# Optimization experiments

Measured on AMD Instinct MI355X. Metric: run time of the kernel, lower is better.

## Reference

```python
import jax, jax.numpy as jnp
import numpy as np
import math

CODE_DIMS = [32, 32]
NUM_CODEBOOK = 16
FEAT_DIM = 1024
EPS = 1e-12


def rms_norm(x, eps=EPS):
    var = jnp.mean(x * x, axis=-1, keepdims=True) + eps
    return x * jax.lax.rsqrt(var)


def outer_product(y, code_dims):
    # y: [..., h, sum(code_dims)] -> [..., h, prod(code_dims)]
    splits = list(np.cumsum(code_dims)[:-1])
    mats = jnp.split(y, splits, axis=-1)
    out = mats[0]
    for m in mats[1:]:
        out = out[..., :, None] * m[..., None, :]
        out = out.reshape(*out.shape[:-2], -1)
    return out


def setup_inputs() -> dict:
    key = jax.random.key(0)
    kx, kw = jax.random.split(key)
    x = jax.random.normal(kx, (4, 2048, FEAT_DIM), dtype=jnp.float32)
    std = math.sqrt(2.0 / (FEAT_DIM + sum(CODE_DIMS)))
    weight = jax.random.normal(kw, (NUM_CODEBOOK, FEAT_DIM, sum(CODE_DIMS)), dtype=jnp.float32) * std
    return {"x": x, "weight": weight}


def reference(x, weight):
    h = weight.shape[0]
    # batched per-codebook linear: [..., d] x [h, d, o] -> [..., h, o]
    y = jnp.einsum('...i,hio->...ho', x, weight)
    # chunked outer product per codebook -> [..., h, prod(code_dims)]
    op = outer_product(y, CODE_DIMS)
    out = jnp.mean(op, axis=-2) * math.sqrt(h)
    return rms_norm(out)
```

## Files before the change

### kernel.cpp

```cpp
#include <hip/hip_runtime.h>
#include <hip/hip_bf16.h>

#define NTOK  8192
#define KDIM  1024
#define NOUT  1024
#define NCB   16

typedef __attribute__((ext_vector_type(8))) short short8;
typedef __attribute__((ext_vector_type(4))) float f32x4;

__device__ static inline unsigned short f2bf(float f) {
    unsigned int u = __float_as_uint(f);
    unsigned int r = (u + 0x7FFFu + ((u >> 16) & 1u)) >> 16;
    return (unsigned short)r;
}

__device__ static inline float bf2f(unsigned int h) {
    return __uint_as_float(h << 16);
}

__device__ static inline void async_copy16(const void* g, void* l) {
    __builtin_amdgcn_global_load_lds(
        (const __attribute__((address_space(1))) void*)g,
        (__attribute__((address_space(3))) void*)l, 16, 0, 0);
}

__global__ __launch_bounds__(256) void conv_x_kernel(const float* __restrict__ x,
                                                     unsigned short* __restrict__ A) {
    int u = blockIdx.x * 256 + threadIdx.x;
    const float* src = x + (size_t)u * 8;
    float4 v0 = *(const float4*)(src);
    float4 v1 = *(const float4*)(src + 4);
    short8 o;
    o[0] = (short)f2bf(v0.x); o[1] = (short)f2bf(v0.y);
    o[2] = (short)f2bf(v0.z); o[3] = (short)f2bf(v0.w);
    o[4] = (short)f2bf(v1.x); o[5] = (short)f2bf(v1.y);
    o[6] = (short)f2bf(v1.z); o[7] = (short)f2bf(v1.w);
    *(short8*)(A + (size_t)u * 8) = o;
}

__global__ __launch_bounds__(256) void conv_w_kernel(const float* __restrict__ W,
                                                     unsigned short* __restrict__ Bt) {
    int u = blockIdx.x * 256 + threadIdx.x;
    int n  = u & (NOUT - 1);
    int k0 = (u >> 10) << 3;
    int h = n >> 6, o = n & 63;
    const float* src = W + (size_t)h * KDIM * 64 + o;
    short8 v;
#pragma unroll
    for (int j = 0; j < 8; ++j)
        v[j] = (short)f2bf(src[(size_t)(k0 + j) * 64]);
    *(short8*)(Bt + (size_t)n * KDIM + k0) = v;
}

__global__ __launch_bounds__(256) void gemm_kernel(const unsigned short* __restrict__ A,
                                                   const unsigned short* __restrict__ Bt,
                                                   unsigned short* __restrict__ Y) {
    __shared__ unsigned short Alds[128 * 32];
    __shared__ unsigned short Blds[128 * 32];

    const int tid = threadIdx.x;
    const int m0 = blockIdx.y * 128;
    const int n0 = blockIdx.x * 128;
    const int lane = tid & 63;
    const int w = tid >> 6;
    const int wr = (w >> 1) * 64;
    const int wc = (w & 1) * 64;
    const int r15 = lane & 15;
    const int kq = (lane >> 4) * 8;

    f32x4 acc[4][4];
#pragma unroll
    for (int m = 0; m < 4; ++m)
#pragma unroll
        for (int n = 0; n < 4; ++n)
            acc[m][n] = (f32x4){0.f, 0.f, 0.f, 0.f};

    const unsigned short* Ag = A + (size_t)m0 * KDIM;
    const unsigned short* Bg = Bt + (size_t)n0 * KDIM;

    for (int kt = 0; kt < KDIM; kt += 32) {
#pragma unroll
        for (int issue = 0; issue < 2; ++issue) {
            int e = (issue * 256 + tid) * 8;
            int row = e >> 5;
            int kk = e & 31;
            async_copy16(Ag + (size_t)row * KDIM + kt + kk, Alds + e);
            async_copy16(Bg + (size_t)row * KDIM + kt + kk, Blds + e);
        }
        __syncthreads();

        short8 af[4], bf[4];
#pragma unroll
        for (int m = 0; m < 4; ++m)
            af[m] = *(const short8*)&Alds[(wr + m * 16 + r15) * 32 + kq];
#pragma unroll
        for (int n = 0; n < 4; ++n)
            bf[n] = *(const short8*)&Blds[(wc + n * 16 + r15) * 32 + kq];

#pragma unroll
        for (int m = 0; m < 4; ++m)
#pragma unroll
            for (int n = 0; n < 4; ++n)
                acc[m][n] = __builtin_amdgcn_mfma_f32_16x16x32_bf16(af[m], bf[n], acc[m][n], 0, 0, 0);
        __syncthreads();
    }

    const int rrow = (lane >> 4) * 4;
#pragma unroll
    for (int m = 0; m < 4; ++m) {
#pragma unroll
        for (int n = 0; n < 4; ++n) {
            int col = n0 + wc + n * 16 + r15;
#pragma unroll
            for (int r = 0; r < 4; ++r) {
                int row = m0 + wr + m * 16 + rrow + r;
                Y[(size_t)row * NOUT + col] = f2bf(acc[m][n][r]);
            }
        }
    }
}

__global__ __launch_bounds__(256) void epilogue_kernel(const unsigned short* __restrict__ Y,
                                                       float* __restrict__ out) {
    __shared__ float ylds[1024];
    __shared__ float red[4];

    const int t = blockIdx.x;
    const int tid = threadIdx.x;
    const unsigned short* yrow = Y + (size_t)t * NOUT;

    {
        uint2 raw = *(const uint2*)(yrow + tid * 4);
        ylds[tid * 4 + 0] = bf2f(raw.x & 0xffffu);
        ylds[tid * 4 + 1] = bf2f(raw.x >> 16);
        ylds[tid * 4 + 2] = bf2f(raw.y & 0xffffu);
        ylds[tid * 4 + 3] = bf2f(raw.y >> 16);
    }
    __syncthreads();

    const int j = tid >> 3;
    const int k0 = (tid & 7) * 4;

    float o0 = 0.f, o1 = 0.f, o2 = 0.f, o3 = 0.f;
#pragma unroll
    for (int h = 0; h < NCB; ++h) {
        float a = ylds[h * 64 + j];
        float4 b = *(const float4*)&ylds[h * 64 + 32 + k0];
        o0 += a * b.x; o1 += a * b.y; o2 += a * b.z; o3 += a * b.w;
    }
    o0 *= 0.25f; o1 *= 0.25f; o2 *= 0.25f; o3 *= 0.25f;

    float ss = o0 * o0 + o1 * o1 + o2 * o2 + o3 * o3;
#pragma unroll
    for (int off = 32; off >= 1; off >>= 1)
        ss += __shfl_xor(ss, off, 64);

    const int lane = tid & 63, w = tid >> 6;
    if (lane == 0) red[w] = ss;
    __syncthreads();
    float tot = red[0] + red[1] + red[2] + red[3];
    float scale = rsqrtf(tot * (1.0f / 1024.0f) + 1e-12f);

    float4 o;
    o.x = o0 * scale; o.y = o1 * scale; o.z = o2 * scale; o.w = o3 * scale;
    *(float4*)(out + (size_t)t * 1024 + tid * 4) = o;
}

extern "C" void kernel_launch(void* const* d_in, const int* in_sizes, int n_in,
                              void* d_out, int out_size, void* d_ws, size_t ws_size,
                              hipStream_t stream) {
    const float* x = (const float*)d_in[0];
    const float* wgt = (const float*)d_in[1];
    float* out = (float*)d_out;

    unsigned short* A  = (unsigned short*)d_ws;
    unsigned short* Bt = (unsigned short*)((char*)d_ws + (16u << 20));
    unsigned short* Y  = (unsigned short*)((char*)d_ws + (18u << 20));

    conv_x_kernel<<<NTOK * KDIM / 8 / 256, 256, 0, stream>>>(x, A);
    conv_w_kernel<<<NOUT * KDIM / 8 / 256, 256, 0, stream>>>(wgt, Bt);
    gemm_kernel<<<dim3(NOUT / 128, NTOK / 128), 256, 0, stream>>>(A, Bt, Y);
    epilogue_kernel<<<NTOK, 256, 0, stream>>>(Y, out);
}
```

Measured before the change: 57.51 us.

## Fuse x conversion, GEMM and outer-product epilogue into one full-width kernel

Replaces the separate x-to-bf16 conversion, tiled GEMM and per-token epilogue with one kernel. Each block computes a 32-token by full-1024-column tile with the B operand double-buffered and XOR-swizzled in LDS, and converts x to bf16 on the fly. The fp32 result stays in LDS for the codebook outer-product mean and RMS norm, which removes the Y round trip through global memory and two launches. In exchange it uses 132KB of LDS per block, giving one block per CU and only 256 blocks, and every block re-streams the whole B matrix from L2.

```diff
diff --git a/kernel.cpp b/kernel.cpp
--- a/kernel.cpp
+++ b/kernel.cpp
@@ -1,42 +1,24 @@
 #include <hip/hip_runtime.h>
 #include <hip/hip_bf16.h>
 
-#define NTOK  8192
 #define KDIM  1024
 #define NOUT  1024
-#define NCB   16
+#define MTILE 32
+#define BK    32
+#define YPAD  1028
 
 typedef __attribute__((ext_vector_type(8))) short short8;
 typedef __attribute__((ext_vector_type(4))) float f32x4;
 
 __device__ static inline unsigned short f2bf(float f) {
     unsigned int u = __float_as_uint(f);
-    unsigned int r = (u + 0x7FFFu + ((u >> 16) & 1u)) >> 16;
-    return (unsigned short)r;
-}
-
-__device__ static inline float bf2f(unsigned int h) {
-    return __uint_as_float(h << 16);
+    return (unsigned short)((u + 0x7FFFu + ((u >> 16) & 1u)) >> 16);
 }
 
 __device__ static inline void async_copy16(const void* g, void* l) {
     __builtin_amdgcn_global_load_lds(
         (const __attribute__((address_space(1))) void*)g,
         (__attribute__((address_space(3))) void*)l, 16, 0, 0);
-}
-
-__global__ __launch_bounds__(256) void conv_x_kernel(const float* __restrict__ x,
-                                                     unsigned short* __restrict__ A) {
-    int u = blockIdx.x * 256 + threadIdx.x;
-    const float* src = x + (size_t)u * 8;
-    float4 v0 = *(const float4*)(src);
-    float4 v1 = *(const float4*)(src + 4);
-    short8 o;
-    o[0] = (short)f2bf(v0.x); o[1] = (short)f2bf(v0.y);
-    o[2] = (short)f2bf(v0.z); o[3] = (short)f2bf(v0.w);
-    o[4] = (short)f2bf(v1.x); o[5] = (short)f2bf(v1.y);
-    o[6] = (short)f2bf(v1.z); o[7] = (short)f2bf(v1.w);
-    *(short8*)(A + (size_t)u * 8) = o;
 }
 
 __global__ __launch_bounds__(256) void conv_w_kernel(const float* __restrict__ W,
@@ -53,133 +35,172 @@
     *(short8*)(Bt + (size_t)n * KDIM + k0) = v;
 }
 
-__global__ __launch_bounds__(256) void gemm_kernel(const unsigned short* __restrict__ A,
-                                                   const unsigned short* __restrict__ Bt,
-                                                   unsigned short* __restrict__ Y) {
-    __shared__ unsigned short Alds[128 * 32];
-    __shared__ unsigned short Blds[128 * 32];
-
-    const int tid = threadIdx.x;
-    const int m0 = blockIdx.y * 128;
-    const int n0 = blockIdx.x * 128;
+__device__ static inline void stage_b(const unsigned short* __restrict__ Bt,
+                                      unsigned short* Bl, int tid, int kt) {
+#pragma unroll
+    for (int i = 0; i < 8; ++i) {
+        int slot  = i * 512 + tid;
+        int row   = slot >> 2;
+        int kksrc = (((slot & 3) ^ ((row >> 1) & 3)) << 3);
+        async_copy16(Bt + (size_t)row * KDIM + kt + kksrc, Bl + (size_t)slot * 8);
+    }
+}
+
+__global__ __launch_bounds__(512) void fused_kernel(const float* __restrict__ x,
+                                                    const unsigned short* __restrict__ Bt,
+                                                    float* __restrict__ out) {
+    extern __shared__ char smem[];
+    unsigned short* Bl = (unsigned short*)smem;
+    unsigned short* Al = (unsigned short*)(smem + 131072);
+    float* ylds = (float*)smem;
+
+    const int tid  = threadIdx.x;
+    const int m0   = blockIdx.x * MTILE;
     const int lane = tid & 63;
-    const int w = tid >> 6;
-    const int wr = (w >> 1) * 64;
-    const int wc = (w & 1) * 64;
-    const int r15 = lane & 15;
-    const int kq = (lane >> 4) * 8;
-
-    f32x4 acc[4][4];
-#pragma unroll
-    for (int m = 0; m < 4; ++m)
-#pragma unroll
-        for (int n = 0; n < 4; ++n)
-            acc[m][n] = (f32x4){0.f, 0.f, 0.f, 0.f};
-
-    const unsigned short* Ag = A + (size_t)m0 * KDIM;
-    const unsigned short* Bg = Bt + (size_t)n0 * KDIM;
-
-    for (int kt = 0; kt < KDIM; kt += 32) {
-#pragma unroll
-        for (int issue = 0; issue < 2; ++issue) {
-            int e = (issue * 256 + tid) * 8;
-            int row = e >> 5;
-            int kk = e & 31;
-            async_copy16(Ag + (size_t)row * KDIM + kt + kk, Alds + e);
-            async_copy16(Bg + (size_t)row * KDIM + kt + kk, Blds + e);
+    const int w    = tid >> 6;
+    const int r15  = lane & 15;
+    const int kq   = (lane >> 4) * 8;
+    const int cl   = kq >> 3;
+
+    f32x4 acc[2][8];
+#pragma unroll
+    for (int mi = 0; mi < 2; ++mi)
+#pragma unroll
+        for (int nf = 0; nf < 8; ++nf)
+            acc[mi][nf] = (f32x4){0.f, 0.f, 0.f, 0.f};
+
+    const bool aload = (tid < 128);
+    const int arow = tid >> 2;
+    const int akk  = (tid & 3) * 8;
+    const float* xsrc = x + (size_t)(m0 + arow) * KDIM + akk;
+
+    stage_b(Bt, Bl, tid, 0);
+    if (aload) {
+        float4 v0 = *(const float4*)xsrc;
+        float4 v1 = *(const float4*)(xsrc + 4);
+        short8 o;
+        o[0]=(short)f2bf(v0.x); o[1]=(short)f2bf(v0.y); o[2]=(short)f2bf(v0.z); o[3]=(short)f2bf(v0.w);
+        o[4]=(short)f2bf(v1.x); o[5]=(short)f2bf(v1.y); o[6]=(short)f2bf(v1.z); o[7]=(short)f2bf(v1.w);
+        *(short8*)(Al + arow * 32 + akk) = o;
+    }
+    __syncthreads();
+
+    for (int t = 0; t < 32; ++t) {
+        const int b = t & 1;
+        float4 v0, v1;
+        if (t < 31) {
+            stage_b(Bt, Bl + (b ^ 1) * 32768, tid, (t + 1) * BK);
+            if (aload) {
+                v0 = *(const float4*)(xsrc + (t + 1) * BK);
+                v1 = *(const float4*)(xsrc + (t + 1) * BK + 4);
+            }
+        }
+        short8 af[2], bfr[8];
+        const unsigned short* Ab = Al + b * 1024;
+        const unsigned short* Bb = Bl + b * 32768;
+#pragma unroll
+        for (int mi = 0; mi < 2; ++mi)
+            af[mi] = *(const short8*)(Ab + (mi * 16 + r15) * 32 + kq);
+#pragma unroll
+        for (int nf = 0; nf < 8; ++nf) {
+            int row  = w * 128 + nf * 16 + r15;
+            int phys = ((cl ^ ((row >> 1) & 3)) << 3);
+            bfr[nf] = *(const short8*)(Bb + row * 32 + phys);
+        }
+#pragma unroll
+        for (int mi = 0; mi < 2; ++mi)
+#pragma unroll
+            for (int nf = 0; nf < 8; ++nf)
+                acc[mi][nf] = __builtin_amdgcn_mfma_f32_16x16x32_bf16(af[mi], bfr[nf], acc[mi][nf], 0, 0, 0);
+        if (t < 31 && aload) {
+            short8 o;
+            o[0]=(short)f2bf(v0.x); o[1]=(short)f2bf(v0.y); o[2]=(short)f2bf(v0.z); o[3]=(short)f2bf(v0.w);
+            o[4]=(short)f2bf(v1.x); o[5]=(short)f2bf(v1.y); o[6]=(short)f2bf(v1.z); o[7]=(short)f2bf(v1.w);
+            *(short8*)(Al + (b ^ 1) * 1024 + arow * 32 + akk) = o;
         }
         __syncthreads();
-
-        short8 af[4], bf[4];
-#pragma unroll
-        for (int m = 0; m < 4; ++m)
-            af[m] = *(const short8*)&Alds[(wr + m * 16 + r15) * 32 + kq];
-#pragma unroll
-        for (int n = 0; n < 4; ++n)
-            bf[n] = *(const short8*)&Blds[(wc + n * 16 + r15) * 32 + kq];
-
-#pragma unroll
-        for (int m = 0; m < 4; ++m)
-#pragma unroll
-            for (int n = 0; n < 4; ++n)
-                acc[m][n] = __builtin_amdgcn_mfma_f32_16x16x32_bf16(af[m], bf[n], acc[m][n], 0, 0, 0);
-        __syncthreads();
-    }
-
-    const int rrow = (lane >> 4) * 4;
-#pragma unroll
-    for (int m = 0; m < 4; ++m) {
-#pragma unroll
-        for (int n = 0; n < 4; ++n) {
-            int col = n0 + wc + n * 16 + r15;
-#pragma unroll
-            for (int r = 0; r < 4; ++r) {
-                int row = m0 + wr + m * 16 + rrow + r;
-                Y[(size_t)row * NOUT + col] = f2bf(acc[m][n][r]);
+    }
+
+    const int rr = (lane >> 4) * 4;
+#pragma unroll
+    for (int mi = 0; mi < 2; ++mi)
+#pragma unroll
+        for (int nf = 0; nf < 8; ++nf) {
+            int col = w * 128 + nf * 16 + r15;
+#pragma unroll
+            for (int r = 0; r < 4; ++r)
+                ylds[(mi * 16 + rr + r) * YPAD + col] = acc[mi][nf][r];
+        }
+    __syncthreads();
+
+    const int tok = tid >> 4;
+    const int q   = tid & 15;
+    const int j0  = (q >> 2) * 8;
+    const int k0  = (q & 3) * 8;
+    const float* yr = ylds + tok * YPAD;
+
+    float o[8][8];
+#pragma unroll
+    for (int j = 0; j < 8; ++j)
+#pragma unroll
+        for (int k = 0; k < 8; ++k) o[j][k] = 0.f;
+
+#pragma unroll
+    for (int h = 0; h < 16; ++h) {
+        float4 a0 = *(const float4*)(yr + h * 64 + j0);
+        float4 a1 = *(const float4*)(yr + h * 64 + j0 + 4);
+        float4 b0 = *(const float4*)(yr + h * 64 + 32 + k0);
+        float4 b1 = *(const float4*)(yr + h * 64 + 32 + k0 + 4);
+        float aa0[4] = {a0.x, a0.y, a0.z, a0.w};
+        float aa1[4] = {a1.x, a1.y, a1.z, a1.w};
+        float bb0[4] = {b0.x, b0.y, b0.z, b0.w};
+        float bb1[4] = {b1.x, b1.y, b1.z, b1.w};
+#pragma unroll
+        for (int j = 0; j < 4; ++j)
+#pragma unroll
+            for (int k = 0; k < 4; ++k) {
+                o[j][k]       += aa0[j] * bb0[k];
+                o[j][k + 4]   += aa0[j] * bb1[k];
+                o[j + 4][k]   += aa1[j] * bb0[k];
+                o[j + 4][k + 4] += aa1[j] * bb1[k];
             }
-        }
-    }
-}
-
-__global__ __launch_bounds__(256) void epilogue_kernel(const unsigned short* __restrict__ Y,
-                                                       float* __restrict__ out) {
-    __shared__ float ylds[1024];
-    __shared__ float red[4];
-
-    const int t = blockIdx.x;
-    const int tid = threadIdx.x;
-    const unsigned short* yrow = Y + (size_t)t * NOUT;
-
-    {
-        uint2 raw = *(const uint2*)(yrow + tid * 4);
-        ylds[tid * 4 + 0] = bf2f(raw.x & 0xffffu);
-        ylds[tid * 4 + 1] = bf2f(raw.x >> 16);
-        ylds[tid * 4 + 2] = bf2f(raw.y & 0xffffu);
-        ylds[tid * 4 + 3] = bf2f(raw.y >> 16);
-    }
-    __syncthreads();
-
-    const int j = tid >> 3;
-    const int k0 = (tid & 7) * 4;
-
-    float o0 = 0.f, o1 = 0.f, o2 = 0.f, o3 = 0.f;
-#pragma unroll
-    for (int h = 0; h < NCB; ++h) {
-        float a = ylds[h * 64 + j];
-        float4 b = *(const float4*)&ylds[h * 64 + 32 + k0];
-        o0 += a * b.x; o1 += a * b.y; o2 += a * b.z; o3 += a * b.w;
-    }
-    o0 *= 0.25f; o1 *= 0.25f; o2 *= 0.25f; o3 *= 0.25f;
-
-    float ss = o0 * o0 + o1 * o1 + o2 * o2 + o3 * o3;
-#pragma unroll
-    for (int off = 32; off >= 1; off >>= 1)
+    }
+
+    float ss = 0.f;
+#pragma unroll
+    for (int j = 0; j < 8; ++j)
+#pragma unroll
+        for (int k = 0; k < 8; ++k) {
+            o[j][k] *= 0.25f;
+            ss += o[j][k] * o[j][k];
+        }
+#pragma unroll
+    for (int off = 1; off < 16; off <<= 1)
         ss += __shfl_xor(ss, off, 64);
-
-    const int lane = tid & 63, w = tid >> 6;
-    if (lane == 0) red[w] = ss;
-    __syncthreads();
-    float tot = red[0] + red[1] + red[2] + red[3];
-    float scale = rsqrtf(tot * (1.0f / 1024.0f) + 1e-12f);
-
-    float4 o;
-    o.x = o0 * scale; o.y = o1 * scale; o.z = o2 * scale; o.w = o3 * scale;
-    *(float4*)(out + (size_t)t * 1024 + tid * 4) = o;
+    const float scale = rsqrtf(ss * (1.0f / 1024.0f) + 1e-12f);
+
+    float* orow = out + (size_t)(m0 + tok) * 1024 + k0;
+#pragma unroll
+    for (int j = 0; j < 8; ++j) {
+        float4 w0, w1;
+        w0.x = o[j][0] * scale; w0.y = o[j][1] * scale; w0.z = o[j][2] * scale; w0.w = o[j][3] * scale;
+        w1.x = o[j][4] * scale; w1.y = o[j][5] * scale; w1.z = o[j][6] * scale; w1.w = o[j][7] * scale;
+        *(float4*)(orow + (j0 + j) * 32)     = w0;
+        *(float4*)(orow + (j0 + j) * 32 + 4) = w1;
+    }
 }
 
 extern "C" void kernel_launch(void* const* d_in, const int* in_sizes, int n_in,
                               void* d_out, int out_size, void* d_ws, size_t ws_size,
                               hipStream_t stream) {
-    const float* x = (const float*)d_in[0];
+    const float* x   = (const float*)d_in[0];
     const float* wgt = (const float*)d_in[1];
     float* out = (float*)d_out;
-
-    unsigned short* A  = (unsigned short*)d_ws;
-    unsigned short* Bt = (unsigned short*)((char*)d_ws + (16u << 20));
-    unsigned short* Y  = (unsigned short*)((char*)d_ws + (18u << 20));
-
-    conv_x_kernel<<<NTOK * KDIM / 8 / 256, 256, 0, stream>>>(x, A);
+    unsigned short* Bt = (unsigned short*)d_ws;
+
+    (void)hipFuncSetAttribute((const void*)fused_kernel,
+                              hipFuncAttributeMaxDynamicSharedMemorySize, 135168);
+
     conv_w_kernel<<<NOUT * KDIM / 8 / 256, 256, 0, stream>>>(wgt, Bt);
-    gemm_kernel<<<dim3(NOUT / 128, NTOK / 128), 256, 0, stream>>>(A, Bt, Y);
-    epilogue_kernel<<<NTOK, 256, 0, stream>>>(Y, out);
-}
+    fused_kernel<<<8192 / MTILE, 512, 135168, stream>>>(x, Bt, out);
+}
```

After: 63.19 us. 1.1x slower.

## Fuse fp32-to-bf16 conversion of x into GEMM with double-buffered swizzled LDS

Applied to the files above, without the earlier changes.

Removes the separate conv_x pass, so the GEMM reads fp32 x directly, converts it to bf16 in registers and writes it into a swizzled LDS tile. LDS is now double-buffered, with the next B tile fetched asynchronously and the next A tile loaded into registers while the current MFMAs run, leaving one barrier per k-step. An XOR swizzle is applied to LDS columns to cut bank conflicts. In exchange, each GEMM block rereads fp32 x (twice the bytes of bf16) for every column tile and does the conversion work redundantly across the 8 column blocks.

```diff
diff --git a/kernel.cpp b/kernel.cpp
--- a/kernel.cpp
+++ b/kernel.cpp
@@ -1,9 +1,9 @@
 #include <hip/hip_runtime.h>
 #include <hip/hip_bf16.h>
 
-#define NTOK  8192
 #define KDIM  1024
 #define NOUT  1024
+#define NTOK  8192
 #define NCB   16
 
 typedef __attribute__((ext_vector_type(8))) short short8;
@@ -11,8 +11,7 @@
 
 __device__ static inline unsigned short f2bf(float f) {
     unsigned int u = __float_as_uint(f);
-    unsigned int r = (u + 0x7FFFu + ((u >> 16) & 1u)) >> 16;
-    return (unsigned short)r;
+    return (unsigned short)((u + 0x7FFFu + ((u >> 16) & 1u)) >> 16);
 }
 
 __device__ static inline float bf2f(unsigned int h) {
@@ -25,18 +24,13 @@
         (__attribute__((address_space(3))) void*)l, 16, 0, 0);
 }
 
-__global__ __launch_bounds__(256) void conv_x_kernel(const float* __restrict__ x,
-                                                     unsigned short* __restrict__ A) {
-    int u = blockIdx.x * 256 + threadIdx.x;
-    const float* src = x + (size_t)u * 8;
-    float4 v0 = *(const float4*)(src);
-    float4 v1 = *(const float4*)(src + 4);
+__device__ static inline short8 cvt8(float4 a, float4 b) {
     short8 o;
-    o[0] = (short)f2bf(v0.x); o[1] = (short)f2bf(v0.y);
-    o[2] = (short)f2bf(v0.z); o[3] = (short)f2bf(v0.w);
-    o[4] = (short)f2bf(v1.x); o[5] = (short)f2bf(v1.y);
-    o[6] = (short)f2bf(v1.z); o[7] = (short)f2bf(v1.w);
-    *(short8*)(A + (size_t)u * 8) = o;
+    o[0] = (short)f2bf(a.x); o[1] = (short)f2bf(a.y);
+    o[2] = (short)f2bf(a.z); o[3] = (short)f2bf(a.w);
+    o[4] = (short)f2bf(b.x); o[5] = (short)f2bf(b.y);
+    o[6] = (short)f2bf(b.z); o[7] = (short)f2bf(b.w);
+    return o;
 }
 
 __global__ __launch_bounds__(256) void conv_w_kernel(const float* __restrict__ W,
@@ -53,21 +47,27 @@
     *(short8*)(Bt + (size_t)n * KDIM + k0) = v;
 }
 
-__global__ __launch_bounds__(256) void gemm_kernel(const unsigned short* __restrict__ A,
-                                                   const unsigned short* __restrict__ Bt,
-                                                   unsigned short* __restrict__ Y) {
-    __shared__ unsigned short Alds[128 * 32];
-    __shared__ unsigned short Blds[128 * 32];
+__global__ __launch_bounds__(256) void gemm_fused_kernel(const float* __restrict__ x,
+                                                         const unsigned short* __restrict__ Bt,
+                                                         unsigned short* __restrict__ Y) {
+    __shared__ unsigned short Bl[2][128 * 32];
+    __shared__ unsigned short Al[2][128 * 32];
 
     const int tid = threadIdx.x;
+    const int n0 = blockIdx.x * 128;
     const int m0 = blockIdx.y * 128;
-    const int n0 = blockIdx.x * 128;
     const int lane = tid & 63;
     const int w = tid >> 6;
     const int wr = (w >> 1) * 64;
     const int wc = (w & 1) * 64;
     const int r15 = lane & 15;
     const int kq = (lane >> 4) * 8;
+    const int cl = kq >> 3;
+
+    const int arow = tid >> 1;
+    const int ac0  = (tid & 1) * 2;
+    const int aswz = (arow >> 1) & 3;
+    const float* xsrc = x + (size_t)(m0 + arow) * KDIM + (tid & 1) * 16;
 
     f32x4 acc[4][4];
 #pragma unroll
@@ -76,33 +76,62 @@
         for (int n = 0; n < 4; ++n)
             acc[m][n] = (f32x4){0.f, 0.f, 0.f, 0.f};
 
-    const unsigned short* Ag = A + (size_t)m0 * KDIM;
-    const unsigned short* Bg = Bt + (size_t)n0 * KDIM;
-
-    for (int kt = 0; kt < KDIM; kt += 32) {
-#pragma unroll
-        for (int issue = 0; issue < 2; ++issue) {
-            int e = (issue * 256 + tid) * 8;
-            int row = e >> 5;
-            int kk = e & 31;
-            async_copy16(Ag + (size_t)row * KDIM + kt + kk, Alds + e);
-            async_copy16(Bg + (size_t)row * KDIM + kt + kk, Blds + e);
-        }
-        __syncthreads();
-
-        short8 af[4], bf[4];
+#pragma unroll
+    for (int i = 0; i < 2; ++i) {
+        int slot = i * 256 + tid;
+        int row = slot >> 2, ch = slot & 3;
+        int ks = ((ch ^ ((row >> 1) & 3)) << 3);
+        async_copy16(Bt + (size_t)(n0 + row) * KDIM + ks, &Bl[0][slot * 8]);
+    }
+    {
+        float4 p0 = *(const float4*)(xsrc);
+        float4 p1 = *(const float4*)(xsrc + 4);
+        float4 p2 = *(const float4*)(xsrc + 8);
+        float4 p3 = *(const float4*)(xsrc + 12);
+        *(short8*)&Al[0][arow * 32 + ((ac0 ^ aswz) << 3)]       = cvt8(p0, p1);
+        *(short8*)&Al[0][arow * 32 + (((ac0 + 1) ^ aswz) << 3)] = cvt8(p2, p3);
+    }
+    __syncthreads();
+
+    for (int t = 0; t < 32; ++t) {
+        const int b = t & 1;
+        float4 p0, p1, p2, p3;
+        if (t < 31) {
+            const int kt = (t + 1) * 32;
+#pragma unroll
+            for (int i = 0; i < 2; ++i) {
+                int slot = i * 256 + tid;
+                int row = slot >> 2, ch = slot & 3;
+                int ks = ((ch ^ ((row >> 1) & 3)) << 3);
+                async_copy16(Bt + (size_t)(n0 + row) * KDIM + kt + ks, &Bl[b ^ 1][slot * 8]);
+            }
+            p0 = *(const float4*)(xsrc + kt);
+            p1 = *(const float4*)(xsrc + kt + 4);
+            p2 = *(const float4*)(xsrc + kt + 8);
+            p3 = *(const float4*)(xsrc + kt + 12);
+        }
+
+        short8 af[4], bfr[4];
+#pragma unroll
+        for (int m = 0; m < 4; ++m) {
+            int ra = wr + m * 16 + r15;
+            af[m] = *(const short8*)&Al[b][ra * 32 + ((cl ^ ((ra >> 1) & 3)) << 3)];
+        }
+#pragma unroll
+        for (int n = 0; n < 4; ++n) {
+            int rb = wc + n * 16 + r15;
+            bfr[n] = *(const short8*)&Bl[b][rb * 32 + ((cl ^ ((rb >> 1) & 3)) << 3)];
+        }
 #pragma unroll
         for (int m = 0; m < 4; ++m)
-            af[m] = *(const short8*)&Alds[(wr + m * 16 + r15) * 32 + kq];
-#pragma unroll
-        for (int n = 0; n < 4; ++n)
-            bf[n] = *(const short8*)&Blds[(wc + n * 16 + r15) * 32 + kq];
-
-#pragma unroll
-        for (int m = 0; m < 4; ++m)
 #pragma unroll
             for (int n = 0; n < 4; ++n)
-                acc[m][n] = __builtin_amdgcn_mfma_f32_16x16x32_bf16(af[m], bf[n], acc[m][n], 0, 0, 0);
+                acc[m][n] = __builtin_amdgcn_mfma_f32_16x16x32_bf16(af[m], bfr[n], acc[m][n], 0, 0, 0);
+
+        if (t < 31) {
+            *(short8*)&Al[b ^ 1][arow * 32 + ((ac0 ^ aswz) << 3)]       = cvt8(p0, p1);
+            *(short8*)&Al[b ^ 1][arow * 32 + (((ac0 + 1) ^ aswz) << 3)] = cvt8(p2, p3);
+        }
         __syncthreads();
     }
 
@@ -146,8 +175,8 @@
 #pragma unroll
     for (int h = 0; h < NCB; ++h) {
         float a = ylds[h * 64 + j];
-        float4 b = *(const float4*)&ylds[h * 64 + 32 + k0];
-        o0 += a * b.x; o1 += a * b.y; o2 += a * b.z; o3 += a * b.w;
+        float4 bb = *(const float4*)&ylds[h * 64 + 32 + k0];
+        o0 += a * bb.x; o1 += a * bb.y; o2 += a * bb.z; o3 += a * bb.w;
     }
     o0 *= 0.25f; o1 *= 0.25f; o2 *= 0.25f; o3 *= 0.25f;
 
@@ -170,16 +199,14 @@
 extern "C" void kernel_launch(void* const* d_in, const int* in_sizes, int n_in,
                               void* d_out, int out_size, void* d_ws, size_t ws_size,
                               hipStream_t stream) {
-    const float* x = (const float*)d_in[0];
+    const float* x   = (const float*)d_in[0];
     const float* wgt = (const float*)d_in[1];
     float* out = (float*)d_out;
 
-    unsigned short* A  = (unsigned short*)d_ws;
-    unsigned short* Bt = (unsigned short*)((char*)d_ws + (16u << 20));
-    unsigned short* Y  = (unsigned short*)((char*)d_ws + (18u << 20));
-
-    conv_x_kernel<<<NTOK * KDIM / 8 / 256, 256, 0, stream>>>(x, A);
+    unsigned short* Bt = (unsigned short*)d_ws;
+    unsigned short* Y  = (unsigned short*)((char*)d_ws + (2u << 20));
+
     conv_w_kernel<<<NOUT * KDIM / 8 / 256, 256, 0, stream>>>(wgt, Bt);
-    gemm_kernel<<<dim3(NOUT / 128, NTOK / 128), 256, 0, stream>>>(A, Bt, Y);
+    gemm_fused_kernel<<<dim3(NOUT / 128, NTOK / 128), 256, 0, stream>>>(x, Bt, Y);
     epilogue_kernel<<<NTOK, 256, 0, stream>>>(Y, out);
 }
```

Result: slower. 68.10 us (+18.4%).

## Replace tiled GEMM with B-stationary LDS kernel streaming A from global

Applied to the files above, without the earlier changes.

Replaces the 128x128 double-syncthreads GEMM with a kernel that loads a full 64-column by K=1024 slice of B into 128KB of dynamic LDS once, using an XOR swizzle. Each of 8 waves then streams 64 rows of A straight from global memory into registers, with a one-step register prefetch and no per-k barriers. Blocks are mapped so each XCD covers contiguous M ranges, to improve L2 locality. The risks: A is re-read across 16 N-tiles, each CU holds only one 512-thread block, and global-load latency is hidden only by a shallow prefetch.

```diff
diff --git a/kernel.cpp b/kernel.cpp
--- a/kernel.cpp
+++ b/kernel.cpp
@@ -1,9 +1,9 @@
 #include <hip/hip_runtime.h>
 #include <hip/hip_bf16.h>
 
-#define NTOK  8192
 #define KDIM  1024
 #define NOUT  1024
+#define NTOK  8192
 #define NCB   16
 
 typedef __attribute__((ext_vector_type(8))) short short8;
@@ -11,8 +11,7 @@
 
 __device__ static inline unsigned short f2bf(float f) {
     unsigned int u = __float_as_uint(f);
-    unsigned int r = (u + 0x7FFFu + ((u >> 16) & 1u)) >> 16;
-    return (unsigned short)r;
+    return (unsigned short)((u + 0x7FFFu + ((u >> 16) & 1u)) >> 16);
 }
 
 __device__ static inline float bf2f(unsigned int h) {
@@ -53,69 +52,100 @@
     *(short8*)(Bt + (size_t)n * KDIM + k0) = v;
 }
 
-__global__ __launch_bounds__(256) void gemm_kernel(const unsigned short* __restrict__ A,
-                                                   const unsigned short* __restrict__ Bt,
-                                                   unsigned short* __restrict__ Y) {
-    __shared__ unsigned short Alds[128 * 32];
-    __shared__ unsigned short Blds[128 * 32];
-
-    const int tid = threadIdx.x;
-    const int m0 = blockIdx.y * 128;
-    const int n0 = blockIdx.x * 128;
+__global__ __launch_bounds__(512, 2) void gemm_bstat_kernel(const unsigned short* __restrict__ A,
+                                                            const unsigned short* __restrict__ Bt,
+                                                            unsigned short* __restrict__ Y) {
+    extern __shared__ unsigned short Blds[];
+
+    const int id  = blockIdx.x;
+    const int xcd = id & 7;
+    const int j   = id >> 3;
+    const int m0  = (xcd * 2 + (j >> 4)) * 512;
+    const int n0  = (j & 15) * 64;
+
+    const int tid  = threadIdx.x;
     const int lane = tid & 63;
-    const int w = tid >> 6;
-    const int wr = (w >> 1) * 64;
-    const int wc = (w & 1) * 64;
-    const int r15 = lane & 15;
-    const int kq = (lane >> 4) * 8;
+    const int w    = tid >> 6;
+    const int r15  = lane & 15;
+    const int q    = lane >> 4;
+    const int kq   = q * 8;
+
+#pragma unroll
+    for (int i = 0; i < 16; ++i) {
+        int slot = i * 512 + tid;
+        int row  = slot >> 7;
+        int cd   = slot & 127;
+        int cs   = cd ^ (row & 7);
+        async_copy16(Bt + (size_t)(n0 + row) * KDIM + cs * 8, Blds + slot * 8);
+    }
+    __syncthreads();
+
+    const unsigned short* Aw = A + (size_t)(m0 + w * 64 + r15) * KDIM + kq;
 
     f32x4 acc[4][4];
 #pragma unroll
-    for (int m = 0; m < 4; ++m)
-#pragma unroll
-        for (int n = 0; n < 4; ++n)
-            acc[m][n] = (f32x4){0.f, 0.f, 0.f, 0.f};
-
-    const unsigned short* Ag = A + (size_t)m0 * KDIM;
-    const unsigned short* Bg = Bt + (size_t)n0 * KDIM;
-
-    for (int kt = 0; kt < KDIM; kt += 32) {
-#pragma unroll
-        for (int issue = 0; issue < 2; ++issue) {
-            int e = (issue * 256 + tid) * 8;
-            int row = e >> 5;
-            int kk = e & 31;
-            async_copy16(Ag + (size_t)row * KDIM + kt + kk, Alds + e);
-            async_copy16(Bg + (size_t)row * KDIM + kt + kk, Blds + e);
+    for (int mf = 0; mf < 4; ++mf)
+#pragma unroll
+        for (int nf = 0; nf < 4; ++nf)
+            acc[mf][nf] = (f32x4){0.f, 0.f, 0.f, 0.f};
+
+    short8 a0[4], a1[4];
+#pragma unroll
+    for (int mf = 0; mf < 4; ++mf) a0[mf] = *(const short8*)(Aw + mf * 16 * KDIM);
+#pragma unroll
+    for (int mf = 0; mf < 4; ++mf) a1[mf] = *(const short8*)(Aw + mf * 16 * KDIM + 32);
+
+#pragma unroll
+    for (int tt = 0; tt < 16; ++tt) {
+        {
+            const int c = 8 * tt + q;
+            short8 bf[4];
+#pragma unroll
+            for (int nf = 0; nf < 4; ++nf) {
+                int ra = nf * 16 + r15;
+                bf[nf] = *(const short8*)&Blds[ra * KDIM + ((c ^ (ra & 7)) << 3)];
+            }
+#pragma unroll
+            for (int mf = 0; mf < 4; ++mf)
+#pragma unroll
+                for (int nf = 0; nf < 4; ++nf)
+                    acc[mf][nf] = __builtin_amdgcn_mfma_f32_16x16x32_bf16(a0[mf], bf[nf], acc[mf][nf], 0, 0, 0);
+            if (tt < 15) {
+#pragma unroll
+                for (int mf = 0; mf < 4; ++mf)
+                    a0[mf] = *(const short8*)(Aw + mf * 16 * KDIM + (tt + 1) * 64);
+            }
         }
-        __syncthreads();
-
-        short8 af[4], bf[4];
-#pragma unroll
-        for (int m = 0; m < 4; ++m)
-            af[m] = *(const short8*)&Alds[(wr + m * 16 + r15) * 32 + kq];
-#pragma unroll
-        for (int n = 0; n < 4; ++n)
-            bf[n] = *(const short8*)&Blds[(wc + n * 16 + r15) * 32 + kq];
-
-#pragma unroll
-        for (int m = 0; m < 4; ++m)
-#pragma unroll
-            for (int n = 0; n < 4; ++n)
-                acc[m][n] = __builtin_amdgcn_mfma_f32_16x16x32_bf16(af[m], bf[n], acc[m][n], 0, 0, 0);
-        __syncthreads();
-    }
-
-    const int rrow = (lane >> 4) * 4;
-#pragma unroll
-    for (int m = 0; m < 4; ++m) {
-#pragma unroll
-        for (int n = 0; n < 4; ++n) {
-            int col = n0 + wc + n * 16 + r15;
+        {
+            const int c = 8 * tt + 4 + q;
+            short8 bf[4];
+#pragma unroll
+            for (int nf = 0; nf < 4; ++nf) {
+                int ra = nf * 16 + r15;
+                bf[nf] = *(const short8*)&Blds[ra * KDIM + ((c ^ (ra & 7)) << 3)];
+            }
+#pragma unroll
+            for (int mf = 0; mf < 4; ++mf)
+#pragma unroll
+                for (int nf = 0; nf < 4; ++nf)
+                    acc[mf][nf] = __builtin_amdgcn_mfma_f32_16x16x32_bf16(a1[mf], bf[nf], acc[mf][nf], 0, 0, 0);
+            if (tt < 15) {
+#pragma unroll
+                for (int mf = 0; mf < 4; ++mf)
+                    a1[mf] = *(const short8*)(Aw + mf * 16 * KDIM + (tt + 1) * 64 + 32);
+            }
+        }
+    }
+
+#pragma unroll
+    for (int mf = 0; mf < 4; ++mf) {
+#pragma unroll
+        for (int nf = 0; nf < 4; ++nf) {
+            int col = n0 + nf * 16 + r15;
 #pragma unroll
             for (int r = 0; r < 4; ++r) {
-                int row = m0 + wr + m * 16 + rrow + r;
-                Y[(size_t)row * NOUT + col] = f2bf(acc[m][n][r]);
+                int row = m0 + w * 64 + mf * 16 + q * 4 + r;
+                Y[(size_t)row * NOUT + col] = f2bf(acc[mf][nf][r]);
             }
         }
     }
@@ -146,8 +176,8 @@
 #pragma unroll
     for (int h = 0; h < NCB; ++h) {
         float a = ylds[h * 64 + j];
-        float4 b = *(const float4*)&ylds[h * 64 + 32 + k0];
-        o0 += a * b.x; o1 += a * b.y; o2 += a * b.z; o3 += a * b.w;
+        float4 bb = *(const float4*)&ylds[h * 64 + 32 + k0];
+        o0 += a * bb.x; o1 += a * bb.y; o2 += a * bb.z; o3 += a * bb.w;
     }
     o0 *= 0.25f; o1 *= 0.25f; o2 *= 0.25f; o3 *= 0.25f;
 
@@ -156,8 +186,8 @@
     for (int off = 32; off >= 1; off >>= 1)
         ss += __shfl_xor(ss, off, 64);
 
-    const int lane = tid & 63, w = tid >> 6;
-    if (lane == 0) red[w] = ss;
+    const int lane = tid & 63, wv = tid >> 6;
+    if (lane == 0) red[wv] = ss;
     __syncthreads();
     float tot = red[0] + red[1] + red[2] + red[3];
     float scale = rsqrtf(tot * (1.0f / 1024.0f) + 1e-12f);
@@ -170,7 +200,7 @@
 extern "C" void kernel_launch(void* const* d_in, const int* in_sizes, int n_in,
                               void* d_out, int out_size, void* d_ws, size_t ws_size,
                               hipStream_t stream) {
-    const float* x = (const float*)d_in[0];
+    const float* x   = (const float*)d_in[0];
     const float* wgt = (const float*)d_in[1];
     float* out = (float*)d_out;
 
@@ -178,8 +208,11 @@
     unsigned short* Bt = (unsigned short*)((char*)d_ws + (16u << 20));
     unsigned short* Y  = (unsigned short*)((char*)d_ws + (18u << 20));
 
+    (void)hipFuncSetAttribute((const void*)gemm_bstat_kernel,
+                              hipFuncAttributeMaxDynamicSharedMemorySize, 131072);
+
     conv_x_kernel<<<NTOK * KDIM / 8 / 256, 256, 0, stream>>>(x, A);
     conv_w_kernel<<<NOUT * KDIM / 8 / 256, 256, 0, stream>>>(wgt, Bt);
-    gemm_kernel<<<dim3(NOUT / 128, NTOK / 128), 256, 0, stream>>>(A, Bt, Y);
+    gemm_bstat_kernel<<<256, 512, 131072, stream>>>(A, Bt, Y);
     epilogue_kernel<<<NTOK, 256, 0, stream>>>(Y, out);
 }
```

New measurement: 65.31 us. 13.6% more time.
